# Performance work log

Hardware: AMD Instinct MI355X
Metric: run time of the kernel (lower is better)

The kernel has to match this reference:

```python
import jax, jax.numpy as jnp
import numpy as np

WIN = 7            # skimage default win_size
K1 = 0.01
K2 = 0.03
DATA_RANGE = 1.0   # images are in [0, 1]
PAD = (WIN - 1) // 2


def _uniform_filter_valid(x):
    # x: [N, 1, H, W] -> valid 7x7 box filter (== skimage uniform_filter cropped by PAD)
    k = jnp.ones((1, 1, WIN, WIN), x.dtype) / (WIN * WIN)
    return jax.lax.conv_general_dilated(
        x, k, window_strides=(1, 1), padding='VALID',
        dimension_numbers=('NCHW', 'OIHW', 'NCHW'))


def _ssim_mean(a, b):
    # a, b: [B, C, H, W]; each [H, W] slice is one independent SSIM image
    B, C, H, W = a.shape
    x = a.reshape(B * C, 1, H, W)
    y = b.reshape(B * C, 1, H, W)

    ux = _uniform_filter_valid(x)
    uy = _uniform_filter_valid(y)
    uxx = _uniform_filter_valid(x * x)
    uyy = _uniform_filter_valid(y * y)
    uxy = _uniform_filter_valid(x * y)

    NP = WIN * WIN
    cov_norm = NP / (NP - 1.0)  # sample covariance correction (skimage default)
    vx = cov_norm * (uxx - ux * ux)
    vy = cov_norm * (uyy - uy * uy)
    vxy = cov_norm * (uxy - ux * uy)

    C1 = (K1 * DATA_RANGE) ** 2
    C2 = (K2 * DATA_RANGE) ** 2

    S = ((2.0 * ux * uy + C1) * (2.0 * vxy + C2)) / \
        ((ux * ux + uy * uy + C1) * (vx + vy + C2))

    # skimage crops PAD border then means; VALID conv already cropped it.
    # All images are the same size, so np.average(per-image means) == global mean.
    return jnp.mean(S)


def setup_inputs() -> dict:
    key = jax.random.key(0)
    k1, k2 = jax.random.split(key)
    pred = jax.random.uniform(k1, (32, 4, 384, 384), dtype=jnp.float32)
    actual = jax.random.uniform(k2, (32, 4, 384, 384), dtype=jnp.float32)
    return {"pred": pred, "actual": actual}


def reference(pred, actual):
    return _ssim_mean(pred, actual)
```

## Files before the change

### kernel.cpp

```cpp
#include <hip/hip_runtime.h>


#define H 384
#define W 384
#define IMGSZ (H * W)
#define OWIDTH 378
#define NIMG 128
#define SY 21
#define NRS 18
#define NCT 7
#define WPI (NRS * NCT)
#define NWAVE (NIMG * WPI)
#define WVPB 4
#define NBLKM (NWAVE / WVPB)

__device__ __forceinline__ float wave_reduce(float v) {
#pragma unroll
    for (int off = 32; off > 0; off >>= 1) v += __shfl_down(v, off, 64);
    return v;
}

__device__ __forceinline__ float win7(float v) {
    const float a = v + __shfl_down(v, 1, 64);
    const float b = a + __shfl_down(a, 2, 64);
    return (b + __shfl_down(a, 4, 64)) + __shfl_down(v, 6, 64);
}

#define STEP(J, S) do {                                                   \
    const float xo = xv[S], yo = yv[S];                                   \
    const float xn = pfx[J], yn = pfy[J];                                 \
    sx += xn - xo; sy += yn - yo;                                         \
    sq = fmaf(xn, xn, fmaf(yn, yn, fmaf(-xo, xo, fmaf(-yo, yo, sq))));    \
    sxy = fmaf(xn, yn, fmaf(-xo, yo, sxy));                               \
    xv[S] = xn; yv[S] = yn;                                               \
    const float Sx = win7(sx), Sy = win7(sy);                             \
    const float Sq = win7(sq), Sxy = win7(sxy);                           \
    const float p  = Sx * Sy;                                             \
    const float qq = fmaf(Sx, Sx, Sy * Sy);                               \
    const float n1 = fmaf(2.f, p, C1B);                                   \
    const float n2 = fmaf(98.f, Sxy, fmaf(-2.f, p, C2B));                 \
    const float d1 = qq + C1B;                                            \
    const float d2 = fmaf(49.f, Sq, C2B - qq);                            \
    const float s  = (n1 * n2) * __builtin_amdgcn_rcpf(d1 * d2);          \
    acc = lok ? acc + s : acc;                                            \
} while (0)

#define BLOCK7 do {                                                       \
    STEP(0, 6); STEP(1, 0); STEP(2, 1); STEP(3, 2);                       \
    STEP(4, 3); STEP(5, 4); STEP(6, 5);                                   \
} while (0)

__global__ __launch_bounds__(256, 8) void ssim_main(const float* __restrict__ pred,
                                                    const float* __restrict__ act,
                                                    float* __restrict__ partials) {
    __shared__ float red[WVPB];

    const int t = threadIdx.x;
    const int lane = t & 63;
    const int w = t >> 6;
    const int wid = blockIdx.x * WVPB + w;
    const int img = wid / WPI;
    const int rem = wid - img * WPI;
    const int rs = rem / NCT;
    const int ct = rem - rs * NCT;

    const int y0 = rs * SY;
    const int c0 = ct * 58;
    const int nc_raw = OWIDTH - c0;
    const int ncols = (nc_raw < 58) ? nc_raw : 58;
    const bool lok = lane < ncols;

    int col = c0 + lane;
    col = (col < W) ? col : (W - 1);
    const float* px = pred + (size_t)img * IMGSZ + (size_t)y0 * W + col;
    const float* py = act  + (size_t)img * IMGSZ + (size_t)y0 * W + col;

    const float C1B = 0.2401f;
    const float C2B = 2.1168f;
    float acc = 0.f;

    float xv[7], yv[7];
#pragma unroll
    for (int i = 0; i < 6; ++i) { xv[i] = px[i * W]; yv[i] = py[i * W]; }
    xv[6] = 0.f; yv[6] = 0.f;
    float sx = 0.f, sy = 0.f, sq = 0.f, sxy = 0.f;
#pragma unroll
    for (int i = 0; i < 6; ++i) {
        sx += xv[i]; sy += yv[i];
        sq = fmaf(xv[i], xv[i], fmaf(yv[i], yv[i], sq));
        sxy = fmaf(xv[i], yv[i], sxy);
    }
    float pfx[7], pfy[7];
#pragma unroll
    for (int i = 0; i < 7; ++i) { pfx[i] = px[(6 + i) * W]; pfy[i] = py[(6 + i) * W]; }

    const float* qx = px + 13 * W;
    const float* qy = py + 13 * W;
#pragma unroll 1
    for (int c = 0; c < 2; ++c) {
        float nfx[7], nfy[7];
#pragma unroll
        for (int i = 0; i < 7; ++i) { nfx[i] = qx[i * W]; nfy[i] = qy[i * W]; }
        qx += 7 * W; qy += 7 * W;
        BLOCK7;
#pragma unroll
        for (int i = 0; i < 7; ++i) { pfx[i] = nfx[i]; pfy[i] = nfy[i]; }
    }
    BLOCK7;

    const float wsum = wave_reduce(acc);
    if (lane == 0) red[w] = wsum;
    __syncthreads();
    if (t == 0) partials[blockIdx.x] = (red[0] + red[1]) + (red[2] + red[3]);
}

__global__ __launch_bounds__(1024) void ssim_finalize(const float* __restrict__ partials,
                                                      float* __restrict__ out) {
    __shared__ double red[1024];
    const int t = threadIdx.x;
    double s = 0.0;
    for (int i = t; i < NBLKM; i += 1024) s += (double)partials[i];
    red[t] = s;
    __syncthreads();
#pragma unroll
    for (int off = 512; off > 0; off >>= 1) {
        if (t < off) red[t] += red[t + off];
        __syncthreads();
    }
    if (t == 0) out[0] = (float)(red[0] / ((double)NIMG * OWIDTH * OWIDTH));
}

extern "C" void kernel_launch(void* const* d_in, const int* in_sizes, int n_in,
                              void* d_out, int out_size, void* d_ws, size_t ws_size,
                              hipStream_t stream) {
    const float* pred = (const float*)d_in[0];
    const float* act  = (const float*)d_in[1];
    float* partials = (float*)d_ws;
    ssim_main<<<NBLKM, 256, 0, stream>>>(pred, act, partials);
    ssim_finalize<<<1, 1024, 0, stream>>>(partials, (float*)d_out);
}
```

Measured before the change: 190.1 us.

## Process two columns per lane with packed float2 math and DPP row shifts

Each lane now handles two adjacent output columns as a float2 vector. The horizontal 7-wide sum uses DPP row-shift-left within 16-lane rows instead of wave-wide shuffles. Each 16-lane group covers a 26-column tile with a 6-column halo, down from the 6-of-64 halo lanes per wave before. This cuts redundant halo lanes, lets the compiler emit packed FP32 ops, and reduces waves per image from 7 to 4 column tiles. The cost is higher register use, so the occupancy hint drops from 8 to 4, and 3 of every 16 lanes still do masked halo work.

```diff
diff --git a/kernel.cpp b/kernel.cpp
--- a/kernel.cpp
+++ b/kernel.cpp
@@ -1,5 +1,7 @@
 #include <hip/hip_runtime.h>
 
+
+typedef float v2f __attribute__((ext_vector_type(2)));
 
 #define H 384
 #define W 384
@@ -7,12 +9,24 @@
 #define OWIDTH 378
 #define NIMG 128
 #define SY 21
-#define NRS 18
-#define NCT 7
-#define WPI (NRS * NCT)
+#define NBANDS 18
+#define NCW 4
+#define WPI (NBANDS * NCW)
 #define NWAVE (NIMG * WPI)
 #define WVPB 4
 #define NBLKM (NWAVE / WVPB)
+
+#define SHL1 0x101
+#define SHL2 0x102
+#define SHL3 0x103
+
+template <int CTRL>
+__device__ __forceinline__ float dshl(float v) {
+    return __int_as_float(__builtin_amdgcn_update_dpp(
+        0, __float_as_int(v), CTRL, 0xF, 0xF, true));
+}
+
+#define FMA2(A, B, C) __builtin_elementwise_fma((A), (B), (C))
 
 __device__ __forceinline__ float wave_reduce(float v) {
 #pragma unroll
@@ -20,29 +34,35 @@
     return v;
 }
 
-__device__ __forceinline__ float win7(float v) {
-    const float a = v + __shfl_down(v, 1, 64);
-    const float b = a + __shfl_down(a, 2, 64);
-    return (b + __shfl_down(a, 4, 64)) + __shfl_down(v, 6, 64);
-}
+#define HOR(S2, O2) do {                                                  \
+    const float p_ = (S2).x + (S2).y;                                     \
+    const float u_ = p_ + dshl<SHL1>(p_);                                 \
+    const float c_ = u_ + dshl<SHL2>(p_);                                 \
+    (O2).x = c_ + dshl<SHL3>((S2).x);                                     \
+    (O2).y = (S2).y + dshl<SHL1>(c_);                                     \
+} while (0)
 
 #define STEP(J, S) do {                                                   \
-    const float xo = xv[S], yo = yv[S];                                   \
-    const float xn = pfx[J], yn = pfy[J];                                 \
-    sx += xn - xo; sy += yn - yo;                                         \
-    sq = fmaf(xn, xn, fmaf(yn, yn, fmaf(-xo, xo, fmaf(-yo, yo, sq))));    \
-    sxy = fmaf(xn, yn, fmaf(-xo, yo, sxy));                               \
-    xv[S] = xn; yv[S] = yn;                                               \
-    const float Sx = win7(sx), Sy = win7(sy);                             \
-    const float Sq = win7(sq), Sxy = win7(sxy);                           \
-    const float p  = Sx * Sy;                                             \
-    const float qq = fmaf(Sx, Sx, Sy * Sy);                               \
-    const float n1 = fmaf(2.f, p, C1B);                                   \
-    const float n2 = fmaf(98.f, Sxy, fmaf(-2.f, p, C2B));                 \
-    const float d1 = qq + C1B;                                            \
-    const float d2 = fmaf(49.f, Sq, C2B - qq);                            \
-    const float s  = (n1 * n2) * __builtin_amdgcn_rcpf(d1 * d2);          \
-    acc = lok ? acc + s : acc;                                            \
+    const v2f xn = pfx[J], yn = pfy[J];                                   \
+    const v2f xo = rx[S],  yo = ry[S];                                    \
+    sx2 += xn - xo;                                                       \
+    sy2 += yn - yo;                                                       \
+    sq2 = FMA2(xn, xn, FMA2(yn, yn, FMA2(-xo, xo, FMA2(-yo, yo, sq2)))); \
+    sw2 = FMA2(xn, yn, FMA2(-xo, yo, sw2));                               \
+    rx[S] = xn; ry[S] = yn;                                               \
+    v2f Sx2, Sy2, Sq2, Sw2;                                               \
+    HOR(sx2, Sx2); HOR(sy2, Sy2); HOR(sq2, Sq2); HOR(sw2, Sw2);           \
+    const v2f p2  = Sx2 * Sy2;                                            \
+    const v2f qq2 = FMA2(Sx2, Sx2, Sy2 * Sy2);                            \
+    const v2f n12 = FMA2((v2f)2.f, p2, (v2f)C1B);                         \
+    const v2f n22 = FMA2((v2f)98.f, Sw2, FMA2((v2f)(-2.f), p2, (v2f)C2B));\
+    const v2f d12 = qq2 + (v2f)C1B;                                       \
+    const v2f d22 = FMA2((v2f)49.f, Sq2, (v2f)C2B - qq2);                 \
+    const v2f den = d12 * d22;                                            \
+    v2f r2;                                                               \
+    r2.x = __builtin_amdgcn_rcpf(den.x);                                  \
+    r2.y = __builtin_amdgcn_rcpf(den.y);                                  \
+    acc2 = FMA2(n12 * n22 * r2, msk2, acc2);                              \
 } while (0)
 
 #define BLOCK7 do {                                                       \
@@ -50,7 +70,7 @@
     STEP(4, 3); STEP(5, 4); STEP(6, 5);                                   \
 } while (0)
 
-__global__ __launch_bounds__(256, 8) void ssim_main(const float* __restrict__ pred,
+__global__ __launch_bounds__(256, 4) void ssim_main(const float* __restrict__ pred,
                                                     const float* __restrict__ act,
                                                     float* __restrict__ partials) {
     __shared__ float red[WVPB];
@@ -61,46 +81,56 @@
     const int wid = blockIdx.x * WVPB + w;
     const int img = wid / WPI;
     const int rem = wid - img * WPI;
-    const int rs = rem / NCT;
-    const int ct = rem - rs * NCT;
+    const int band = rem >> 2;
+    const int cw = rem & 3;
+    const int l = lane & 15;
+    const int g = lane >> 4;
+    const int tile = cw * 4 + g;
+    const int ca = tile * 26 + 2 * l;
+    const bool oka = (l <= 12) && (ca < OWIDTH);
+    const bool okb = (l <= 12) && (ca + 1 < OWIDTH);
+    v2f msk2; msk2.x = oka ? 1.f : 0.f; msk2.y = okb ? 1.f : 0.f;
+    const int coff = (ca < 382) ? ca : 382;
+    const int y0 = band * SY;
 
-    const int y0 = rs * SY;
-    const int c0 = ct * 58;
-    const int nc_raw = OWIDTH - c0;
-    const int ncols = (nc_raw < 58) ? nc_raw : 58;
-    const bool lok = lane < ncols;
-
-    int col = c0 + lane;
-    col = (col < W) ? col : (W - 1);
-    const float* px = pred + (size_t)img * IMGSZ + (size_t)y0 * W + col;
-    const float* py = act  + (size_t)img * IMGSZ + (size_t)y0 * W + col;
+    const float* bx = pred + (size_t)img * IMGSZ + (size_t)y0 * W + coff;
+    const float* by = act  + (size_t)img * IMGSZ + (size_t)y0 * W + coff;
 
     const float C1B = 0.2401f;
     const float C2B = 2.1168f;
-    float acc = 0.f;
 
-    float xv[7], yv[7];
-#pragma unroll
-    for (int i = 0; i < 6; ++i) { xv[i] = px[i * W]; yv[i] = py[i * W]; }
-    xv[6] = 0.f; yv[6] = 0.f;
-    float sx = 0.f, sy = 0.f, sq = 0.f, sxy = 0.f;
+    v2f rx[7], ry[7];
 #pragma unroll
     for (int i = 0; i < 6; ++i) {
-        sx += xv[i]; sy += yv[i];
-        sq = fmaf(xv[i], xv[i], fmaf(yv[i], yv[i], sq));
-        sxy = fmaf(xv[i], yv[i], sxy);
+        rx[i] = *(const v2f*)(bx + i * W);
+        ry[i] = *(const v2f*)(by + i * W);
     }
-    float pfx[7], pfy[7];
+    rx[6] = (v2f)0.f; ry[6] = (v2f)0.f;
+    v2f sx2 = (v2f)0.f, sy2 = (v2f)0.f, sq2 = (v2f)0.f, sw2 = (v2f)0.f;
 #pragma unroll
-    for (int i = 0; i < 7; ++i) { pfx[i] = px[(6 + i) * W]; pfy[i] = py[(6 + i) * W]; }
+    for (int i = 0; i < 6; ++i) {
+        sx2 += rx[i]; sy2 += ry[i];
+        sq2 = FMA2(rx[i], rx[i], FMA2(ry[i], ry[i], sq2));
+        sw2 = FMA2(rx[i], ry[i], sw2);
+    }
+    v2f pfx[7], pfy[7];
+#pragma unroll
+    for (int i = 0; i < 7; ++i) {
+        pfx[i] = *(const v2f*)(bx + (6 + i) * W);
+        pfy[i] = *(const v2f*)(by + (6 + i) * W);
+    }
+    v2f acc2 = (v2f)0.f;
 
-    const float* qx = px + 13 * W;
-    const float* qy = py + 13 * W;
+    const float* qx = bx + 13 * W;
+    const float* qy = by + 13 * W;
 #pragma unroll 1
     for (int c = 0; c < 2; ++c) {
-        float nfx[7], nfy[7];
+        v2f nfx[7], nfy[7];
 #pragma unroll
-        for (int i = 0; i < 7; ++i) { nfx[i] = qx[i * W]; nfy[i] = qy[i * W]; }
+        for (int i = 0; i < 7; ++i) {
+            nfx[i] = *(const v2f*)(qx + i * W);
+            nfy[i] = *(const v2f*)(qy + i * W);
+        }
         qx += 7 * W; qy += 7 * W;
         BLOCK7;
 #pragma unroll
@@ -108,7 +138,7 @@
     }
     BLOCK7;
 
-    const float wsum = wave_reduce(acc);
+    const float wsum = wave_reduce(acc2.x + acc2.y);
     if (lane == 0) red[w] = wsum;
     __syncthreads();
     if (t == 0) partials[blockIdx.x] = (red[0] + red[1]) + (red[2] + red[3]);
```

Measured after the change: 166.7 us. 12.3% less time.
